# Kernel optimization log

Measured on AMD Instinct MI355X. Metric: run time of the kernel, lower is better.

Reference implementation:

```python
import jax, jax.numpy as jnp
import numpy as np

BN_EPS = 1e-5

def setup_inputs() -> dict:
    key = jax.random.key(0)
    ks = jax.random.split(key, 5)
    B, C, H, W = 4, 64, 64, 64
    s = 1.0 / np.sqrt(C)
    return {
        "x": jax.random.normal(ks[0], (B, C, H, W), dtype=jnp.float32),
        "Wk": jax.random.normal(ks[1], (C, C), dtype=jnp.float32) * s,
        "Wq": jax.random.normal(ks[2], (C, C), dtype=jnp.float32) * s,
        "Wv": jax.random.normal(ks[3], (C, C), dtype=jnp.float32) * s,
        "W2": jax.random.normal(ks[4], (C, C), dtype=jnp.float32) * s,
        "gamma": jnp.ones((C,), dtype=jnp.float32),
        "beta": jnp.zeros((C,), dtype=jnp.float32),
        "running_mean": jnp.zeros((C,), dtype=jnp.float32),
        "running_var": jnp.ones((C,), dtype=jnp.float32),
    }

def reference(x, Wk, Wq, Wv, W2, gamma, beta, running_mean, running_var):
    B, C, H, W = x.shape
    N = H * W
    xf = x.reshape(B, C, N)                      # flatten spatial -> (B,C,N)
    # 1x1 convs (no bias) == channel matmuls
    k = jnp.einsum('oc,bcn->bon', Wk, xf)        # (B,C,N)
    q = jnp.einsum('oc,bcn->bon', Wq, xf)
    v = jnp.einsum('oc,bcn->bon', Wv, xf)
    # scores[b,n,m] = sum_c k[b,c,n] * q[b,c,m]  (note: no 1/sqrt(d) scaling, as in source)
    scores = jnp.einsum('bcn,bcm->bnm', k, q)    # (B,N,N)
    p = jax.nn.softmax(scores, axis=2)
    # att[b,c,n] = sum_m p[b,n,m] * v[b,c,m]
    att = jnp.einsum('bnm,bcm->bcn', p, v)       # (B,C,N)
    y = jnp.einsum('oc,bcn->bon', W2, att)       # 1x1 conv
    inv = gamma / jnp.sqrt(running_var + BN_EPS)
    y = y * inv[None, :, None] + (beta - running_mean * inv)[None, :, None]
    y = jax.nn.relu(y)
    return y.reshape(B, C, H, W) + x
```

## Files before the change

### kernel.cpp

```cpp
#include <hip/hip_runtime.h>

#define CH   64
#define NTOT 4096
#define NB   4
#define L2E  1.44269504088896340736f

typedef short  short4v  __attribute__((ext_vector_type(4)));
typedef short  short8v  __attribute__((ext_vector_type(8)));
typedef float  floatx4  __attribute__((ext_vector_type(4)));

static __device__ __forceinline__ unsigned pk2bf(float lo, float hi) {
    unsigned r;
    asm("v_cvt_pk_bf16_f32 %0, %1, %2" : "=v"(r) : "v"(lo), "v"(hi));
    return r;
}

static __device__ __forceinline__ float ex2(float x) {
    return __builtin_amdgcn_exp2f(x);
}

__global__ __launch_bounds__(256) void qkv_proj(
    const float* __restrict__ x,
    const float* __restrict__ Wk, const float* __restrict__ Wq,
    const float* __restrict__ Wv,
    short* __restrict__ kT, short* __restrict__ qT, short* __restrict__ vg)
{
    __shared__ __align__(16) float xs [64][36];
    __shared__ __align__(16) float wkT[64][68];
    __shared__ __align__(16) float wqT[64][68];
    __shared__ __align__(16) float wvT[64][68];

    const int tid = threadIdx.x;
    const int b  = blockIdx.x >> 7;
    const int n0 = (blockIdx.x & 127) * 32;
    const float* xb = x + (size_t)b * CH * NTOT;

    {
        int c = tid >> 2, nn = (tid & 3) << 3;
        *(float4*)&xs[c][nn]     = *(const float4*)&xb[(size_t)c * NTOT + n0 + nn];
        *(float4*)&xs[c][nn + 4] = *(const float4*)&xb[(size_t)c * NTOT + n0 + nn + 4];
    }
    for (int i = tid; i < 64 * 64; i += 256) {
        int o = i >> 6, c = i & 63;
        wkT[c][o] = Wk[i];
        wqT[c][o] = Wq[i];
        wvT[c][o] = Wv[i];
    }
    __syncthreads();

    const int to = tid >> 4, tn = tid & 15;
    const int ob = to * 4, nb = tn * 2;
    float ak[4][2] = {}, aq[4][2] = {}, av[4][2] = {};

    for (int c = 0; c < 64; ++c) {
        float x0 = xs[c][nb], x1 = xs[c][nb + 1];
        float4 k4 = *(const float4*)&wkT[c][ob];
        float4 q4 = *(const float4*)&wqT[c][ob];
        float4 v4 = *(const float4*)&wvT[c][ob];
        float ka[4] = {k4.x, k4.y, k4.z, k4.w};
        float qa[4] = {q4.x, q4.y, q4.z, q4.w};
        float va[4] = {v4.x, v4.y, v4.z, v4.w};
        #pragma unroll
        for (int i = 0; i < 4; ++i) {
            ak[i][0] += ka[i] * x0;  ak[i][1] += ka[i] * x1;
            aq[i][0] += qa[i] * x0;  aq[i][1] += qa[i] * x1;
            av[i][0] += va[i] * x0;  av[i][1] += va[i] * x1;
        }
    }

    #pragma unroll
    for (int j = 0; j < 2; ++j) {
        size_t row = (size_t)(b << 12) + n0 + nb + j;
        uint2 kk, qq;
        kk.x = pk2bf(ak[0][j], ak[1][j]);
        kk.y = pk2bf(ak[2][j], ak[3][j]);
        qq.x = pk2bf(aq[0][j], aq[1][j]);
        qq.y = pk2bf(aq[2][j], aq[3][j]);
        *(uint2*)&kT[row * 64 + ob] = kk;
        *(uint2*)&qT[row * 64 + ob] = qq;
    }
    #pragma unroll
    for (int i = 0; i < 4; ++i)
        *(unsigned*)&vg[(((size_t)(b << 6) + ob + i) << 12) + n0 + nb] =
            pk2bf(av[i][0], av[i][1]);
}

__global__ __launch_bounds__(256) void attn_partial(
    const short* __restrict__ kT, const short* __restrict__ qT,
    const short* __restrict__ vg,
    float* __restrict__ opart, float* __restrict__ mlpart)
{
    __shared__ __align__(16) short smem[18432];

    const int tid = threadIdx.x;
    const int w  = tid >> 6;
    const int l  = tid & 63;
    const int g  = l >> 4;
    const int ln = l & 15;

    const int bid  = blockIdx.x;
    const int xcd  = bid & 7, grp = bid >> 3;
    const int bk   = (xcd << 1) | (grp >> 6);
    const int b    = bk >> 2;
    const int kc   = bk & 3;
    const int qblk = grp & 63;
    const int part = (b << 8) | (kc << 6) | qblk;
    const int n0   = qblk << 6;
    const int kbase = kc << 10;

    const short* kTb = kT + ((size_t)(b << 12) + n0) * 64;
    const short* qTb = qT + ((size_t)b << 12) * 64;
    const short* vb  = vg + ((size_t)(b << 6) << 12);

    short* const kTs = smem;
    short* const qS  = smem + 4608;
    short* const vS  = smem + 9216;
    short* const PsW = smem + 13824 + w * 1152;

    {
        int r0 = tid >> 3, c8 = (tid & 7) << 3;
        *(short8v*)&kTs[r0 * 72 + c8]        = *(const short8v*)&kTb[r0 * 64 + c8];
        *(short8v*)&kTs[(r0 + 32) * 72 + c8] = *(const short8v*)&kTb[(r0 + 32) * 64 + c8];
    }
    __syncthreads();

    short8v bS0 = *(const short8v*)&kTs[((w << 4) + ln) * 72 + (g << 3)];
    short8v bS1 = *(const short8v*)&kTs[((w << 4) + ln) * 72 + 32 + (g << 3)];

    float mrun = -1e30f;
    float lrun = 0.f;
    floatx4 acc_o[4];
    #pragma unroll
    for (int ct = 0; ct < 4; ++ct) acc_o[ct] = (floatx4){0.f, 0.f, 0.f, 0.f};

    const int i0 = tid, i1 = tid + 256;

    short8v pf[4];
    pf[0] = *(const short8v*)&qTb[(size_t)(kbase + (i0 >> 3)) * 64 + ((i0 & 7) << 3)];
    pf[1] = *(const short8v*)&qTb[(size_t)(kbase + (i1 >> 3)) * 64 + ((i1 & 7) << 3)];
    pf[2] = *(const short8v*)&vb[(size_t)(i0 >> 3) * 4096 + kbase + ((i0 & 7) << 3)];
    pf[3] = *(const short8v*)&vb[(size_t)(i1 >> 3) * 4096 + kbase + ((i1 & 7) << 3)];

    for (int t = 0; t < 16; ++t) {
        __syncthreads();
        *(short8v*)&qS[(i0 >> 3) * 72 + ((i0 & 7) << 3)] = pf[0];
        *(short8v*)&qS[(i1 >> 3) * 72 + ((i1 & 7) << 3)] = pf[1];
        *(short8v*)&vS[(i0 >> 3) * 72 + ((i0 & 7) << 3)] = pf[2];
        *(short8v*)&vS[(i1 >> 3) * 72 + ((i1 & 7) << 3)] = pf[3];
        __syncthreads();
        if (t < 15) {
            int m1 = kbase + ((t + 1) << 6);
            pf[0] = *(const short8v*)&qTb[(size_t)(m1 + (i0 >> 3)) * 64 + ((i0 & 7) << 3)];
            pf[1] = *(const short8v*)&qTb[(size_t)(m1 + (i1 >> 3)) * 64 + ((i1 & 7) << 3)];
            pf[2] = *(const short8v*)&vb[(size_t)(i0 >> 3) * 4096 + m1 + ((i0 & 7) << 3)];
            pf[3] = *(const short8v*)&vb[(size_t)(i1 >> 3) * 4096 + m1 + ((i1 & 7) << 3)];
        }

        floatx4 sacc[4];
        #pragma unroll
        for (int mt = 0; mt < 4; ++mt) {
            short8v a0 = *(const short8v*)&qS[((mt << 4) + ln) * 72 + (g << 3)];
            short8v a1 = *(const short8v*)&qS[((mt << 4) + ln) * 72 + 32 + (g << 3)];
            floatx4 acc = (floatx4){0.f, 0.f, 0.f, 0.f};
            acc = __builtin_amdgcn_mfma_f32_16x16x32_bf16(a0, bS0, acc, 0, 0, 0);
            acc = __builtin_amdgcn_mfma_f32_16x16x32_bf16(a1, bS1, acc, 0, 0, 0);
            sacc[mt] = acc;
        }

        float mx = sacc[0][0];
        #pragma unroll
        for (int mt = 0; mt < 4; ++mt)
            #pragma unroll
            for (int r = 0; r < 4; ++r) mx = fmaxf(mx, sacc[mt][r]);
        mx = fmaxf(mx, __shfl_xor(mx, 16));
        mx = fmaxf(mx, __shfl_xor(mx, 32));

        if (!__all(mx <= mrun)) {
            float mnew = fmaxf(mrun, mx);
            float fs = ex2((mrun - mnew) * L2E);
            mrun = mnew;
            lrun *= fs;
            #pragma unroll
            for (int ct = 0; ct < 4; ++ct) {
                acc_o[ct][0] *= fs; acc_o[ct][1] *= fs;
                acc_o[ct][2] *= fs; acc_o[ct][3] *= fs;
            }
        }

        const float nm = -mrun * L2E;
        float s = 0.f;
        #pragma unroll
        for (int mt = 0; mt < 4; ++mt) {
            float p0 = ex2(__builtin_fmaf(sacc[mt][0], L2E, nm));
            float p1 = ex2(__builtin_fmaf(sacc[mt][1], L2E, nm));
            float p2 = ex2(__builtin_fmaf(sacc[mt][2], L2E, nm));
            float p3 = ex2(__builtin_fmaf(sacc[mt][3], L2E, nm));
            s += (p0 + p1) + (p2 + p3);
            uint2 pkv;
            pkv.x = pk2bf(p0, p1);
            pkv.y = pk2bf(p2, p3);
            *(uint2*)&PsW[ln * 72 + (mt << 4) + (g << 2)] = pkv;
        }
        s += __shfl_xor(s, 16);
        s += __shfl_xor(s, 32);
        lrun += s;

        short8v bp0 = *(const short8v*)&PsW[ln * 72 + (g << 3)];
        short8v bp1 = *(const short8v*)&PsW[ln * 72 + 32 + (g << 3)];
        #pragma unroll
        for (int ct = 0; ct < 4; ++ct) {
            short8v a0 = *(const short8v*)&vS[((ct << 4) + ln) * 72 + (g << 3)];
            short8v a1 = *(const short8v*)&vS[((ct << 4) + ln) * 72 + 32 + (g << 3)];
            acc_o[ct] = __builtin_amdgcn_mfma_f32_16x16x32_bf16(a0, bp0, acc_o[ct], 0, 0, 0);
            acc_o[ct] = __builtin_amdgcn_mfma_f32_16x16x32_bf16(a1, bp1, acc_o[ct], 0, 0, 0);
        }
    }

    __syncthreads();
    float* xp = (float*)(smem + 4608);
    #pragma unroll
    for (int ct = 0; ct < 4; ++ct)
        #pragma unroll
        for (int r = 0; r < 4; ++r)
            xp[((w << 4) + ln) * 68 + (ct << 4) + (g << 2) + r] = acc_o[ct][r];
    if (g == 0) {
        mlpart[(size_t)part * 128 + (w << 4) + ln]      = mrun;
        mlpart[(size_t)part * 128 + 64 + (w << 4) + ln] = lrun;
    }
    __syncthreads();
    {
        int q = tid >> 2, c16 = (tid & 3) << 4;
        float* Ob = opart + (size_t)part * 4096 + q * 64 + c16;
        #pragma unroll
        for (int i = 0; i < 4; ++i)
            *(float4*)&Ob[i << 2] = *(const float4*)&xp[q * 68 + c16 + (i << 2)];
    }
}

__global__ __launch_bounds__(256) void attn_merge(
    const float* __restrict__ opart, const float* __restrict__ mlpart,
    const float* __restrict__ W2,
    const float* __restrict__ gamma, const float* __restrict__ beta,
    const float* __restrict__ rmean, const float* __restrict__ rvar,
    const float* __restrict__ x, float* __restrict__ out)
{
    __shared__ __align__(16) short attL[64 * 72];
    __shared__ __align__(16) short w2s [64 * 72];
    __shared__ float wgt[4][64];
    __shared__ float linv[64];

    const int tid = threadIdx.x;
    const int w  = tid >> 6;
    const int l  = tid & 63;
    const int g  = l >> 4;
    const int ln = l & 15;

    const int b    = blockIdx.x >> 6;
    const int qblk = blockIdx.x & 63;
    const int n0   = qblk << 6;
    const int part0 = (b << 8) | qblk;

    if (tid < 64) {
        float m0 = mlpart[(size_t)(part0)        * 128 + tid];
        float m1 = mlpart[(size_t)(part0 + 64)   * 128 + tid];
        float m2 = mlpart[(size_t)(part0 + 128)  * 128 + tid];
        float m3 = mlpart[(size_t)(part0 + 192)  * 128 + tid];
        float l0 = mlpart[(size_t)(part0)        * 128 + 64 + tid];
        float l1 = mlpart[(size_t)(part0 + 64)   * 128 + 64 + tid];
        float l2 = mlpart[(size_t)(part0 + 128)  * 128 + 64 + tid];
        float l3 = mlpart[(size_t)(part0 + 192)  * 128 + 64 + tid];
        float mm = fmaxf(fmaxf(m0, m1), fmaxf(m2, m3));
        float w0 = ex2((m0 - mm) * L2E), w1 = ex2((m1 - mm) * L2E);
        float w2 = ex2((m2 - mm) * L2E), w3 = ex2((m3 - mm) * L2E);
        wgt[0][tid] = w0; wgt[1][tid] = w1; wgt[2][tid] = w2; wgt[3][tid] = w3;
        linv[tid] = 1.0f / (w0 * l0 + w1 * l1 + w2 * l2 + w3 * l3);
    }
    for (int i = tid; i < 1024; i += 256) {
        int r = i >> 4, c4 = (i & 15) << 2;
        float4 wv = *(const float4*)&W2[(r << 6) + c4];
        uint2 s4;
        s4.x = pk2bf(wv.x, wv.y);
        s4.y = pk2bf(wv.z, wv.w);
        *(uint2*)&w2s[r * 72 + c4] = s4;
    }
    __syncthreads();

    {
        int q = tid >> 2, c16 = (tid & 3) << 4;
        float a[16] = {};
        #pragma unroll
        for (int kc = 0; kc < 4; ++kc) {
            float wk = wgt[kc][q];
            const float* Ob = opart + (size_t)(part0 + (kc << 6)) * 4096 + q * 64 + c16;
            #pragma unroll
            for (int i = 0; i < 4; ++i) {
                float4 o4 = *(const float4*)&Ob[i << 2];
                a[(i << 2) + 0] += wk * o4.x;
                a[(i << 2) + 1] += wk * o4.y;
                a[(i << 2) + 2] += wk * o4.z;
                a[(i << 2) + 3] += wk * o4.w;
            }
        }
        float li = linv[q];
        #pragma unroll
        for (int i = 0; i < 4; ++i) {
            uint2 s4;
            s4.x = pk2bf(a[(i << 2) + 0] * li, a[(i << 2) + 1] * li);
            s4.y = pk2bf(a[(i << 2) + 2] * li, a[(i << 2) + 3] * li);
            *(uint2*)&attL[q * 72 + c16 + (i << 2)] = s4;
        }
    }
    __syncthreads();

    short8v bA0 = *(const short8v*)&attL[((w << 4) + ln) * 72 + (g << 3)];
    short8v bA1 = *(const short8v*)&attL[((w << 4) + ln) * 72 + 32 + (g << 3)];
    const int nq = n0 + (w << 4) + ln;
    #pragma unroll
    for (int ot = 0; ot < 4; ++ot) {
        short8v a0 = *(const short8v*)&w2s[((ot << 4) + ln) * 72 + (g << 3)];
        short8v a1 = *(const short8v*)&w2s[((ot << 4) + ln) * 72 + 32 + (g << 3)];
        floatx4 acc = (floatx4){0.f, 0.f, 0.f, 0.f};
        acc = __builtin_amdgcn_mfma_f32_16x16x32_bf16(a0, bA0, acc, 0, 0, 0);
        acc = __builtin_amdgcn_mfma_f32_16x16x32_bf16(a1, bA1, acc, 0, 0, 0);
        int o0 = (ot << 4) + (g << 2);
        float4 gm = *(const float4*)&gamma[o0];
        float4 bt = *(const float4*)&beta [o0];
        float4 rm = *(const float4*)&rmean[o0];
        float4 rv = *(const float4*)&rvar [o0];
        float gma[4] = {gm.x, gm.y, gm.z, gm.w};
        float bta[4] = {bt.x, bt.y, bt.z, bt.w};
        float rma[4] = {rm.x, rm.y, rm.z, rm.w};
        float rva[4] = {rv.x, rv.y, rv.z, rv.w};
        #pragma unroll
        for (int r = 0; r < 4; ++r) {
            float inv  = gma[r] * __frsqrt_rn(rva[r] + 1e-5f);
            float bias = bta[r] - rma[r] * inv;
            size_t ga = (((size_t)(b << 6) + o0 + r) << 12) + nq;
            out[ga] = fmaxf(acc[r] * inv + bias, 0.f) + x[ga];
        }
    }
}

extern "C" void kernel_launch(void* const* d_in, const int* in_sizes, int n_in,
                              void* d_out, int out_size, void* d_ws, size_t ws_size,
                              hipStream_t stream)
{
    const float* x     = (const float*)d_in[0];
    const float* Wk    = (const float*)d_in[1];
    const float* Wq    = (const float*)d_in[2];
    const float* Wv    = (const float*)d_in[3];
    const float* W2    = (const float*)d_in[4];
    const float* gamma = (const float*)d_in[5];
    const float* beta  = (const float*)d_in[6];
    const float* rmean = (const float*)d_in[7];
    const float* rvar  = (const float*)d_in[8];
    float* out = (float*)d_out;

    const size_t plane = (size_t)NB * NTOT * CH;
    short* kT = (short*)d_ws;
    short* qT = kT + plane;
    short* vv = qT + plane;
    float* opart  = (float*)(vv + plane);
    float* mlpart = opart + (size_t)1024 * 4096;

    qkv_proj    <<<dim3(512),  dim3(256), 0, stream>>>(x, Wk, Wq, Wv, kT, qT, vv);
    attn_partial<<<dim3(1024), dim3(256), 0, stream>>>(kT, qT, vv, opart, mlpart);
    attn_merge  <<<dim3(256),  dim3(256), 0, stream>>>(opart, mlpart, W2, gamma, beta,
                                                       rmean, rvar, x, out);
}
```

Measured before the change: 69.28 us.

## Double attention query tile per wave and use split-bf16 MFMA for QKV projection

```diff
diff --git a/kernel.cpp b/kernel.cpp
--- a/kernel.cpp
+++ b/kernel.cpp
@@ -14,75 +14,122 @@
     asm("v_cvt_pk_bf16_f32 %0, %1, %2" : "=v"(r) : "v"(lo), "v"(hi));
     return r;
 }
-
 static __device__ __forceinline__ float ex2(float x) {
     return __builtin_amdgcn_exp2f(x);
 }
-
-__global__ __launch_bounds__(256) void qkv_proj(
+static __device__ __forceinline__ short f2bf(float f) {
+    union { float f; unsigned u; } v; v.f = f;
+    unsigned r = v.u + 0x7FFFu + ((v.u >> 16) & 1u);
+    return (short)(r >> 16);
+}
+static __device__ __forceinline__ float bf2f(short s) {
+    union { unsigned u; float f; } v; v.u = ((unsigned)(unsigned short)s) << 16;
+    return v.f;
+}
+
+__global__ __launch_bounds__(256) void qkv_mfma(
     const float* __restrict__ x,
     const float* __restrict__ Wk, const float* __restrict__ Wq,
     const float* __restrict__ Wv,
     short* __restrict__ kT, short* __restrict__ qT, short* __restrict__ vg)
 {
-    __shared__ __align__(16) float xs [64][36];
-    __shared__ __align__(16) float wkT[64][68];
-    __shared__ __align__(16) float wqT[64][68];
-    __shared__ __align__(16) float wvT[64][68];
+    __shared__ __align__(16) short xhi[64 * 72];
+    __shared__ __align__(16) short xlo[64 * 72];
+    __shared__ __align__(16) short whi[64 * 72];
+    __shared__ __align__(16) short wlo[64 * 72];
 
     const int tid = threadIdx.x;
-    const int b  = blockIdx.x >> 7;
-    const int n0 = (blockIdx.x & 127) * 32;
-    const float* xb = x + (size_t)b * CH * NTOT;
-
-    {
-        int c = tid >> 2, nn = (tid & 3) << 3;
-        *(float4*)&xs[c][nn]     = *(const float4*)&xb[(size_t)c * NTOT + n0 + nn];
-        *(float4*)&xs[c][nn + 4] = *(const float4*)&xb[(size_t)c * NTOT + n0 + nn + 4];
-    }
-    for (int i = tid; i < 64 * 64; i += 256) {
-        int o = i >> 6, c = i & 63;
-        wkT[c][o] = Wk[i];
-        wqT[c][o] = Wq[i];
-        wvT[c][o] = Wv[i];
-    }
-    __syncthreads();
-
-    const int to = tid >> 4, tn = tid & 15;
-    const int ob = to * 4, nb = tn * 2;
-    float ak[4][2] = {}, aq[4][2] = {}, av[4][2] = {};
-
-    for (int c = 0; c < 64; ++c) {
-        float x0 = xs[c][nb], x1 = xs[c][nb + 1];
-        float4 k4 = *(const float4*)&wkT[c][ob];
-        float4 q4 = *(const float4*)&wqT[c][ob];
-        float4 v4 = *(const float4*)&wvT[c][ob];
-        float ka[4] = {k4.x, k4.y, k4.z, k4.w};
-        float qa[4] = {q4.x, q4.y, q4.z, q4.w};
-        float va[4] = {v4.x, v4.y, v4.z, v4.w};
-        #pragma unroll
-        for (int i = 0; i < 4; ++i) {
-            ak[i][0] += ka[i] * x0;  ak[i][1] += ka[i] * x1;
-            aq[i][0] += qa[i] * x0;  aq[i][1] += qa[i] * x1;
-            av[i][0] += va[i] * x0;  av[i][1] += va[i] * x1;
-        }
-    }
-
-    #pragma unroll
-    for (int j = 0; j < 2; ++j) {
-        size_t row = (size_t)(b << 12) + n0 + nb + j;
-        uint2 kk, qq;
-        kk.x = pk2bf(ak[0][j], ak[1][j]);
-        kk.y = pk2bf(ak[2][j], ak[3][j]);
-        qq.x = pk2bf(aq[0][j], aq[1][j]);
-        qq.y = pk2bf(aq[2][j], aq[3][j]);
-        *(uint2*)&kT[row * 64 + ob] = kk;
-        *(uint2*)&qT[row * 64 + ob] = qq;
-    }
-    #pragma unroll
-    for (int i = 0; i < 4; ++i)
-        *(unsigned*)&vg[(((size_t)(b << 6) + ob + i) << 12) + n0 + nb] =
-            pk2bf(av[i][0], av[i][1]);
+    const int w = tid >> 6, l = tid & 63, g = l >> 4, ln = l & 15;
+    const int b  = blockIdx.x >> 6;
+    const int n0 = (blockIdx.x & 63) << 6;
+    const float* xb = x + ((size_t)b << 18);
+
+    #pragma unroll
+    for (int i = 0; i < 4; ++i) {
+        int idx = tid + (i << 8);
+        int c = idx >> 4, n4 = (idx & 15) << 2;
+        float4 xv = *(const float4*)&xb[c * 4096 + n0 + n4];
+        float xa[4] = {xv.x, xv.y, xv.z, xv.w};
+        #pragma unroll
+        for (int j = 0; j < 4; ++j) {
+            short h = f2bf(xa[j]);
+            xhi[(n4 + j) * 72 + c] = h;
+            xlo[(n4 + j) * 72 + c] = f2bf(xa[j] - bf2f(h));
+        }
+    }
+
+    const int wo = tid >> 2, wc = (tid & 3) << 4;
+    #pragma unroll
+    for (int j2 = 0; j2 < 4; ++j2) {
+        float4 a = *(const float4*)&Wk[wo * 64 + wc + (j2 << 2)];
+        float aa[4] = {a.x, a.y, a.z, a.w};
+        #pragma unroll
+        for (int j = 0; j < 4; ++j) {
+            short h = f2bf(aa[j]);
+            whi[wo * 72 + wc + (j2 << 2) + j] = h;
+            wlo[wo * 72 + wc + (j2 << 2) + j] = f2bf(aa[j] - bf2f(h));
+        }
+    }
+    __syncthreads();
+
+    short8v xh0 = *(const short8v*)&xhi[((w << 4) + ln) * 72 + (g << 3)];
+    short8v xh1 = *(const short8v*)&xhi[((w << 4) + ln) * 72 + 32 + (g << 3)];
+    short8v xl0 = *(const short8v*)&xlo[((w << 4) + ln) * 72 + (g << 3)];
+    short8v xl1 = *(const short8v*)&xlo[((w << 4) + ln) * 72 + 32 + (g << 3)];
+
+    #pragma unroll
+    for (int m = 0; m < 3; ++m) {
+        if (m > 0) {
+            const float* W = (m == 1) ? Wq : Wv;
+            #pragma unroll
+            for (int j2 = 0; j2 < 4; ++j2) {
+                float4 a = *(const float4*)&W[wo * 64 + wc + (j2 << 2)];
+                float aa[4] = {a.x, a.y, a.z, a.w};
+                #pragma unroll
+                for (int j = 0; j < 4; ++j) {
+                    short h = f2bf(aa[j]);
+                    whi[wo * 72 + wc + (j2 << 2) + j] = h;
+                    wlo[wo * 72 + wc + (j2 << 2) + j] = f2bf(aa[j] - bf2f(h));
+                }
+            }
+            __syncthreads();
+        }
+
+        #pragma unroll
+        for (int ot = 0; ot < 4; ++ot) {
+            short8v ah0 = *(const short8v*)&whi[((ot << 4) + ln) * 72 + (g << 3)];
+            short8v ah1 = *(const short8v*)&whi[((ot << 4) + ln) * 72 + 32 + (g << 3)];
+            short8v al0 = *(const short8v*)&wlo[((ot << 4) + ln) * 72 + (g << 3)];
+            short8v al1 = *(const short8v*)&wlo[((ot << 4) + ln) * 72 + 32 + (g << 3)];
+            floatx4 acc = (floatx4){0.f, 0.f, 0.f, 0.f};
+            if (m < 2) {
+                acc = __builtin_amdgcn_mfma_f32_16x16x32_bf16(ah0, xh0, acc, 0, 0, 0);
+                acc = __builtin_amdgcn_mfma_f32_16x16x32_bf16(ah1, xh1, acc, 0, 0, 0);
+                acc = __builtin_amdgcn_mfma_f32_16x16x32_bf16(al0, xh0, acc, 0, 0, 0);
+                acc = __builtin_amdgcn_mfma_f32_16x16x32_bf16(al1, xh1, acc, 0, 0, 0);
+                acc = __builtin_amdgcn_mfma_f32_16x16x32_bf16(ah0, xl0, acc, 0, 0, 0);
+                acc = __builtin_amdgcn_mfma_f32_16x16x32_bf16(ah1, xl1, acc, 0, 0, 0);
+                short* dst = ((m == 0) ? kT : qT) + ((size_t)b << 18);
+                uint2 p;
+                p.x = pk2bf(acc[0], acc[1]);
+                p.y = pk2bf(acc[2], acc[3]);
+                *(uint2*)&dst[(size_t)(n0 + (w << 4) + ln) * 64 + (ot << 4) + (g << 2)] = p;
+            } else {
+                acc = __builtin_amdgcn_mfma_f32_16x16x32_bf16(xh0, ah0, acc, 0, 0, 0);
+                acc = __builtin_amdgcn_mfma_f32_16x16x32_bf16(xh1, ah1, acc, 0, 0, 0);
+                acc = __builtin_amdgcn_mfma_f32_16x16x32_bf16(xl0, ah0, acc, 0, 0, 0);
+                acc = __builtin_amdgcn_mfma_f32_16x16x32_bf16(xl1, ah1, acc, 0, 0, 0);
+                acc = __builtin_amdgcn_mfma_f32_16x16x32_bf16(xh0, al0, acc, 0, 0, 0);
+                acc = __builtin_amdgcn_mfma_f32_16x16x32_bf16(xh1, al1, acc, 0, 0, 0);
+                short* dst = vg + ((size_t)b << 18);
+                uint2 p;
+                p.x = pk2bf(acc[0], acc[1]);
+                p.y = pk2bf(acc[2], acc[3]);
+                *(uint2*)&dst[(size_t)((ot << 4) + ln) * 4096 + n0 + (w << 4) + (g << 2)] = p;
+            }
+        }
+        __syncthreads();
+    }
 }
 
 __global__ __launch_bounds__(256) void attn_partial(
@@ -90,48 +137,49 @@
     const short* __restrict__ vg,
     float* __restrict__ opart, float* __restrict__ mlpart)
 {
-    __shared__ __align__(16) short smem[18432];
+    __shared__ __align__(16) short smem[27648];
 
     const int tid = threadIdx.x;
-    const int w  = tid >> 6;
-    const int l  = tid & 63;
-    const int g  = l >> 4;
-    const int ln = l & 15;
-
-    const int bid  = blockIdx.x;
-    const int xcd  = bid & 7, grp = bid >> 3;
-    const int bk   = (xcd << 1) | (grp >> 6);
-    const int b    = bk >> 2;
-    const int kc   = bk & 3;
-    const int qblk = grp & 63;
-    const int part = (b << 8) | (kc << 6) | qblk;
-    const int n0   = qblk << 6;
+    const int w = tid >> 6, l = tid & 63, g = l >> 4, ln = l & 15;
+
+    const int bid = blockIdx.x;
+    const int xcd = bid & 7, grp = bid >> 3;
+    const int bk  = (xcd << 1) | (grp >> 5);
+    const int b   = bk >> 2, kc = bk & 3;
+    const int qblk = grp & 31;
+    const int n0   = qblk << 7;
+    const int part = (((b << 2) | kc) << 5) | qblk;
     const int kbase = kc << 10;
 
-    const short* kTb = kT + ((size_t)(b << 12) + n0) * 64;
-    const short* qTb = qT + ((size_t)b << 12) * 64;
-    const short* vb  = vg + ((size_t)(b << 6) << 12);
+    const short* kTb = kT + ((size_t)b << 18) + (size_t)n0 * 64;
+    const short* qTb = qT + ((size_t)b << 18);
+    const short* vb  = vg + ((size_t)b << 18);
 
     short* const kTs = smem;
-    short* const qS  = smem + 4608;
-    short* const vS  = smem + 9216;
-    short* const PsW = smem + 13824 + w * 1152;
-
-    {
-        int r0 = tid >> 3, c8 = (tid & 7) << 3;
-        *(short8v*)&kTs[r0 * 72 + c8]        = *(const short8v*)&kTb[r0 * 64 + c8];
-        *(short8v*)&kTs[(r0 + 32) * 72 + c8] = *(const short8v*)&kTb[(r0 + 32) * 64 + c8];
-    }
-    __syncthreads();
-
-    short8v bS0 = *(const short8v*)&kTs[((w << 4) + ln) * 72 + (g << 3)];
-    short8v bS1 = *(const short8v*)&kTs[((w << 4) + ln) * 72 + 32 + (g << 3)];
-
-    float mrun = -1e30f;
-    float lrun = 0.f;
-    floatx4 acc_o[4];
-    #pragma unroll
-    for (int ct = 0; ct < 4; ++ct) acc_o[ct] = (floatx4){0.f, 0.f, 0.f, 0.f};
+    short* const qS  = smem + 9216;
+    short* const vS  = smem + 13824;
+    short* const PsW = smem + 18432 + w * 2304;
+
+    #pragma unroll
+    for (int j = 0; j < 4; ++j) {
+        int row = tid >> 1, c8 = ((tid & 1) << 5) + (j << 3);
+        *(short8v*)&kTs[row * 72 + c8] = *(const short8v*)&kTb[row * 64 + c8];
+    }
+    __syncthreads();
+
+    short8v bS0 = *(const short8v*)&kTs[((w << 5) + ln) * 72 + (g << 3)];
+    short8v bS1 = *(const short8v*)&kTs[((w << 5) + ln) * 72 + 32 + (g << 3)];
+    short8v bS2 = *(const short8v*)&kTs[((w << 5) + 16 + ln) * 72 + (g << 3)];
+    short8v bS3 = *(const short8v*)&kTs[((w << 5) + 16 + ln) * 72 + 32 + (g << 3)];
+
+    float mrun0 = -1e30f, lrun0 = 0.f;
+    float mrun1 = -1e30f, lrun1 = 0.f;
+    floatx4 acc0[4], acc1[4];
+    #pragma unroll
+    for (int ct = 0; ct < 4; ++ct) {
+        acc0[ct] = (floatx4){0.f, 0.f, 0.f, 0.f};
+        acc1[ct] = (floatx4){0.f, 0.f, 0.f, 0.f};
+    }
 
     const int i0 = tid, i1 = tid + 256;
 
@@ -156,7 +204,7 @@
             pf[3] = *(const short8v*)&vb[(size_t)(i1 >> 3) * 4096 + m1 + ((i1 & 7) << 3)];
         }
 
-        floatx4 sacc[4];
+        floatx4 s0[4], s1[4];
         #pragma unroll
         for (int mt = 0; mt < 4; ++mt) {
             short8v a0 = *(const short8v*)&qS[((mt << 4) + ln) * 72 + (g << 3)];
@@ -164,76 +212,126 @@
             floatx4 acc = (floatx4){0.f, 0.f, 0.f, 0.f};
             acc = __builtin_amdgcn_mfma_f32_16x16x32_bf16(a0, bS0, acc, 0, 0, 0);
             acc = __builtin_amdgcn_mfma_f32_16x16x32_bf16(a1, bS1, acc, 0, 0, 0);
-            sacc[mt] = acc;
-        }
-
-        float mx = sacc[0][0];
-        #pragma unroll
-        for (int mt = 0; mt < 4; ++mt)
-            #pragma unroll
-            for (int r = 0; r < 4; ++r) mx = fmaxf(mx, sacc[mt][r]);
-        mx = fmaxf(mx, __shfl_xor(mx, 16));
-        mx = fmaxf(mx, __shfl_xor(mx, 32));
-
-        if (!__all(mx <= mrun)) {
-            float mnew = fmaxf(mrun, mx);
-            float fs = ex2((mrun - mnew) * L2E);
-            mrun = mnew;
-            lrun *= fs;
-            #pragma unroll
-            for (int ct = 0; ct < 4; ++ct) {
-                acc_o[ct][0] *= fs; acc_o[ct][1] *= fs;
-                acc_o[ct][2] *= fs; acc_o[ct][3] *= fs;
-            }
-        }
-
-        const float nm = -mrun * L2E;
-        float s = 0.f;
-        #pragma unroll
-        for (int mt = 0; mt < 4; ++mt) {
-            float p0 = ex2(__builtin_fmaf(sacc[mt][0], L2E, nm));
-            float p1 = ex2(__builtin_fmaf(sacc[mt][1], L2E, nm));
-            float p2 = ex2(__builtin_fmaf(sacc[mt][2], L2E, nm));
-            float p3 = ex2(__builtin_fmaf(sacc[mt][3], L2E, nm));
-            s += (p0 + p1) + (p2 + p3);
-            uint2 pkv;
-            pkv.x = pk2bf(p0, p1);
-            pkv.y = pk2bf(p2, p3);
-            *(uint2*)&PsW[ln * 72 + (mt << 4) + (g << 2)] = pkv;
-        }
-        s += __shfl_xor(s, 16);
-        s += __shfl_xor(s, 32);
-        lrun += s;
+            s0[mt] = acc;
+            acc = (floatx4){0.f, 0.f, 0.f, 0.f};
+            acc = __builtin_amdgcn_mfma_f32_16x16x32_bf16(a0, bS2, acc, 0, 0, 0);
+            acc = __builtin_amdgcn_mfma_f32_16x16x32_bf16(a1, bS3, acc, 0, 0, 0);
+            s1[mt] = acc;
+        }
+
+        {
+            float mx = s0[0][0];
+            #pragma unroll
+            for (int mt = 0; mt < 4; ++mt)
+                #pragma unroll
+                for (int r = 0; r < 4; ++r) mx = fmaxf(mx, s0[mt][r]);
+            mx = fmaxf(mx, __shfl_xor(mx, 16));
+            mx = fmaxf(mx, __shfl_xor(mx, 32));
+            if (!__all(mx <= mrun0)) {
+                float mnew = fmaxf(mrun0, mx);
+                float fs = ex2((mrun0 - mnew) * L2E);
+                mrun0 = mnew;
+                lrun0 *= fs;
+                #pragma unroll
+                for (int ct = 0; ct < 4; ++ct) {
+                    acc0[ct][0] *= fs; acc0[ct][1] *= fs;
+                    acc0[ct][2] *= fs; acc0[ct][3] *= fs;
+                }
+            }
+            const float nm = -mrun0 * L2E;
+            float s = 0.f;
+            #pragma unroll
+            for (int mt = 0; mt < 4; ++mt) {
+                float p0 = ex2(__builtin_fmaf(s0[mt][0], L2E, nm));
+                float p1 = ex2(__builtin_fmaf(s0[mt][1], L2E, nm));
+                float p2 = ex2(__builtin_fmaf(s0[mt][2], L2E, nm));
+                float p3 = ex2(__builtin_fmaf(s0[mt][3], L2E, nm));
+                s += (p0 + p1) + (p2 + p3);
+                uint2 pkv;
+                pkv.x = pk2bf(p0, p1);
+                pkv.y = pk2bf(p2, p3);
+                *(uint2*)&PsW[ln * 72 + (mt << 4) + (g << 2)] = pkv;
+            }
+            s += __shfl_xor(s, 16);
+            s += __shfl_xor(s, 32);
+            lrun0 += s;
+        }
+        {
+            float mx = s1[0][0];
+            #pragma unroll
+            for (int mt = 0; mt < 4; ++mt)
+                #pragma unroll
+                for (int r = 0; r < 4; ++r) mx = fmaxf(mx, s1[mt][r]);
+            mx = fmaxf(mx, __shfl_xor(mx, 16));
+            mx = fmaxf(mx, __shfl_xor(mx, 32));
+            if (!__all(mx <= mrun1)) {
+                float mnew = fmaxf(mrun1, mx);
+                float fs = ex2((mrun1 - mnew) * L2E);
+                mrun1 = mnew;
+                lrun1 *= fs;
+                #pragma unroll
+                for (int ct = 0; ct < 4; ++ct) {
+                    acc1[ct][0] *= fs; acc1[ct][1] *= fs;
+                    acc1[ct][2] *= fs; acc1[ct][3] *= fs;
+                }
+            }
+            const float nm = -mrun1 * L2E;
+            float s = 0.f;
+            #pragma unroll
+            for (int mt = 0; mt < 4; ++mt) {
+                float p0 = ex2(__builtin_fmaf(s1[mt][0], L2E, nm));
+                float p1 = ex2(__builtin_fmaf(s1[mt][1], L2E, nm));
+                float p2 = ex2(__builtin_fmaf(s1[mt][2], L2E, nm));
+                float p3 = ex2(__builtin_fmaf(s1[mt][3], L2E, nm));
+                s += (p0 + p1) + (p2 + p3);
+                uint2 pkv;
+                pkv.x = pk2bf(p0, p1);
+                pkv.y = pk2bf(p2, p3);
+                *(uint2*)&PsW[(16 + ln) * 72 + (mt << 4) + (g << 2)] = pkv;
+            }
+            s += __shfl_xor(s, 16);
+            s += __shfl_xor(s, 32);
+            lrun1 += s;
+        }
 
         short8v bp0 = *(const short8v*)&PsW[ln * 72 + (g << 3)];
         short8v bp1 = *(const short8v*)&PsW[ln * 72 + 32 + (g << 3)];
+        short8v bp2 = *(const short8v*)&PsW[(16 + ln) * 72 + (g << 3)];
+        short8v bp3 = *(const short8v*)&PsW[(16 + ln) * 72 + 32 + (g << 3)];
         #pragma unroll
         for (int ct = 0; ct < 4; ++ct) {
             short8v a0 = *(const short8v*)&vS[((ct << 4) + ln) * 72 + (g << 3)];
             short8v a1 = *(const short8v*)&vS[((ct << 4) + ln) * 72 + 32 + (g << 3)];
-            acc_o[ct] = __builtin_amdgcn_mfma_f32_16x16x32_bf16(a0, bp0, acc_o[ct], 0, 0, 0);
-            acc_o[ct] = __builtin_amdgcn_mfma_f32_16x16x32_bf16(a1, bp1, acc_o[ct], 0, 0, 0);
-        }
-    }
-
-    __syncthreads();
-    float* xp = (float*)(smem + 4608);
+            acc0[ct] = __builtin_amdgcn_mfma_f32_16x16x32_bf16(a0, bp0, acc0[ct], 0, 0, 0);
+            acc0[ct] = __builtin_amdgcn_mfma_f32_16x16x32_bf16(a1, bp1, acc0[ct], 0, 0, 0);
+            acc1[ct] = __builtin_amdgcn_mfma_f32_16x16x32_bf16(a0, bp2, acc1[ct], 0, 0, 0);
+            acc1[ct] = __builtin_amdgcn_mfma_f32_16x16x32_bf16(a1, bp3, acc1[ct], 0, 0, 0);
+        }
+    }
+
+    __syncthreads();
+    float* xp = (float*)(smem + 9216);
     #pragma unroll
     for (int ct = 0; ct < 4; ++ct)
         #pragma unroll
-        for (int r = 0; r < 4; ++r)
-            xp[((w << 4) + ln) * 68 + (ct << 4) + (g << 2) + r] = acc_o[ct][r];
+        for (int r = 0; r < 4; ++r) {
+            xp[((w << 5) + ln) * 68 + (ct << 4) + (g << 2) + r]      = acc0[ct][r];
+            xp[((w << 5) + 16 + ln) * 68 + (ct << 4) + (g << 2) + r] = acc1[ct][r];
+        }
     if (g == 0) {
-        mlpart[(size_t)part * 128 + (w << 4) + ln]      = mrun;
-        mlpart[(size_t)part * 128 + 64 + (w << 4) + ln] = lrun;
+        mlpart[(size_t)part * 256 + (w << 5) + ln]            = mrun0;
+        mlpart[(size_t)part * 256 + (w << 5) + 16 + ln]       = mrun1;
+        mlpart[(size_t)part * 256 + 128 + (w << 5) + ln]      = lrun0;
+        mlpart[(size_t)part * 256 + 128 + (w << 5) + 16 + ln] = lrun1;
     }
     __syncthreads();
     {
-        int q = tid >> 2, c16 = (tid & 3) << 4;
-        float* Ob = opart + (size_t)part * 4096 + q * 64 + c16;
-        #pragma unroll
-        for (int i = 0; i < 4; ++i)
-            *(float4*)&Ob[i << 2] = *(const float4*)&xp[q * 68 + c16 + (i << 2)];
+        int q = tid >> 1, c32 = (tid & 1) << 5;
+        float* Ob = opart + (size_t)part * 8192 + q * 64 + c32;
+        const float* Xp = &xp[q * 68 + c32];
+        #pragma unroll
+        for (int j = 0; j < 8; ++j)
+            *(float4*)&Ob[j << 2] = *(const float4*)&Xp[j << 2];
     }
 }
 
@@ -250,30 +348,31 @@
     __shared__ float linv[64];
 
     const int tid = threadIdx.x;
-    const int w  = tid >> 6;
-    const int l  = tid & 63;
-    const int g  = l >> 4;
-    const int ln = l & 15;
-
-    const int b    = blockIdx.x >> 6;
-    const int qblk = blockIdx.x & 63;
-    const int n0   = qblk << 6;
-    const int part0 = (b << 8) | qblk;
+    const int w = tid >> 6, l = tid & 63, g = l >> 4, ln = l & 15;
+
+    const int b      = blockIdx.x >> 6;
+    const int qblk64 = blockIdx.x & 63;
+    const int n0     = qblk64 << 6;
+    const int qb128  = qblk64 >> 1;
+    const int qoff   = (qblk64 & 1) << 6;
 
     if (tid < 64) {
-        float m0 = mlpart[(size_t)(part0)        * 128 + tid];
-        float m1 = mlpart[(size_t)(part0 + 64)   * 128 + tid];
-        float m2 = mlpart[(size_t)(part0 + 128)  * 128 + tid];
-        float m3 = mlpart[(size_t)(part0 + 192)  * 128 + tid];
-        float l0 = mlpart[(size_t)(part0)        * 128 + 64 + tid];
-        float l1 = mlpart[(size_t)(part0 + 64)   * 128 + 64 + tid];
-        float l2 = mlpart[(size_t)(part0 + 128)  * 128 + 64 + tid];
-        float l3 = mlpart[(size_t)(part0 + 192)  * 128 + 64 + tid];
-        float mm = fmaxf(fmaxf(m0, m1), fmaxf(m2, m3));
-        float w0 = ex2((m0 - mm) * L2E), w1 = ex2((m1 - mm) * L2E);
-        float w2 = ex2((m2 - mm) * L2E), w3 = ex2((m3 - mm) * L2E);
-        wgt[0][tid] = w0; wgt[1][tid] = w1; wgt[2][tid] = w2; wgt[3][tid] = w3;
-        linv[tid] = 1.0f / (w0 * l0 + w1 * l1 + w2 * l2 + w3 * l3);
+        float mv[4], lv[4];
+        #pragma unroll
+        for (int kc = 0; kc < 4; ++kc) {
+            int part = (((b << 2) | kc) << 5) | qb128;
+            mv[kc] = mlpart[(size_t)part * 256 + qoff + tid];
+            lv[kc] = mlpart[(size_t)part * 256 + 128 + qoff + tid];
+        }
+        float mm = fmaxf(fmaxf(mv[0], mv[1]), fmaxf(mv[2], mv[3]));
+        float den = 0.f;
+        #pragma unroll
+        for (int kc = 0; kc < 4; ++kc) {
+            float wk = ex2((mv[kc] - mm) * L2E);
+            wgt[kc][tid] = wk;
+            den += wk * lv[kc];
+        }
+        linv[tid] = 1.0f / den;
     }
     for (int i = tid; i < 1024; i += 256) {
         int r = i >> 4, c4 = (i & 15) << 2;
@@ -290,8 +389,9 @@
         float a[16] = {};
         #pragma unroll
         for (int kc = 0; kc < 4; ++kc) {
+            int part = (((b << 2) | kc) << 5) | qb128;
             float wk = wgt[kc][q];
-            const float* Ob = opart + (size_t)(part0 + (kc << 6)) * 4096 + q * 64 + c16;
+            const float* Ob = opart + (size_t)part * 8192 + (qoff + q) * 64 + c16;
             #pragma unroll
             for (int i = 0; i < 4; ++i) {
                 float4 o4 = *(const float4*)&Ob[i << 2];
@@ -361,10 +461,10 @@
     short* qT = kT + plane;
     short* vv = qT + plane;
     float* opart  = (float*)(vv + plane);
-    float* mlpart = opart + (size_t)1024 * 4096;
-
-    qkv_proj    <<<dim3(512),  dim3(256), 0, stream>>>(x, Wk, Wq, Wv, kT, qT, vv);
-    attn_partial<<<dim3(1024), dim3(256), 0, stream>>>(kT, qT, vv, opart, mlpart);
-    attn_merge  <<<dim3(256),  dim3(256), 0, stream>>>(opart, mlpart, W2, gamma, beta,
-                                                       rmean, rvar, x, out);
-}
+    float* mlpart = opart + (size_t)512 * 8192;
+
+    qkv_mfma    <<<dim3(256), dim3(256), 0, stream>>>(x, Wk, Wq, Wv, kT, qT, vv);
+    attn_partial<<<dim3(512), dim3(256), 0, stream>>>(kT, qT, vv, opart, mlpart);
+    attn_merge  <<<dim3(256), dim3(256), 0, stream>>>(opart, mlpart, W2, gamma, beta,
+                                                      rmean, rvar, x, out);
+}
```

Measured after the change: 62.88 us. 9.2% less time.
